# Kernel optimization log

Measured on AMD Instinct MI355X. Metric: run time of the kernel, lower is better.

## Reference

```python
import jax, jax.numpy as jnp
import numpy as np

N = 4096        # number of sparse voxel tokens (single sequence)
C = 1024        # channels
H = 16          # num_heads
D = C // H      # head_dim = 64
FREQ_DIM = D // 2 // 3   # 10 rotary freqs per spatial axis
PAD = D // 2 - 3 * FREQ_DIM  # 2 identity-padded complex pairs


def setup_inputs() -> dict:
    key = jax.random.key(0)
    ks = jax.random.split(key, 6)
    s_in = 1.0 / np.sqrt(C)
    x = jax.random.normal(ks[0], (N, C), jnp.float32)
    coords = jax.random.randint(ks[1], (N, 3), 0, 64, dtype=jnp.int32)
    W_qkv = jax.random.normal(ks[2], (C, 3 * C), jnp.float32) * s_in
    b_qkv = jnp.zeros((3 * C,), jnp.float32)
    gamma_q = jnp.ones((H, D), jnp.float32)
    gamma_k = jnp.ones((H, D), jnp.float32)
    W_out = jax.random.normal(ks[3], (C, C), jnp.float32) * s_in
    b_out = jnp.zeros((C,), jnp.float32)
    return {"x": x, "coords": coords, "W_qkv": W_qkv, "b_qkv": b_qkv,
            "gamma_q": gamma_q, "gamma_k": gamma_k, "W_out": W_out, "b_out": b_out}


def _rms_norm(t, gamma):
    # F.normalize(x, dim=-1) * gamma * sqrt(D), computed in fp32
    t = t.astype(jnp.float32)
    nrm = jnp.maximum(jnp.linalg.norm(t, axis=-1, keepdims=True), 1e-12)
    return (t / nrm) * gamma * np.float32(np.sqrt(D))


def _rope_phases(coords):
    # freqs: rope_freq[0] / rope_freq[1]**(i/freq_dim)
    freqs = 1.0 / (10000.0 ** (jnp.arange(FREQ_DIM, dtype=jnp.float32) / FREQ_DIM))
    ph = coords.astype(jnp.float32).reshape(-1)[:, None] * freqs   # [N*3, FREQ_DIM]
    ph = ph.reshape(N, 3 * FREQ_DIM)
    # pad with zero-phase (identity rotation) to head_dim//2
    cos = jnp.concatenate([jnp.cos(ph), jnp.ones((N, PAD), jnp.float32)], axis=-1)
    sin = jnp.concatenate([jnp.sin(ph), jnp.zeros((N, PAD), jnp.float32)], axis=-1)
    return cos, sin


def _rope_apply(t, cos, sin):
    # complex rotation on consecutive pairs of the head dim
    tr = t.reshape(N, H, D // 2, 2)
    t0, t1 = tr[..., 0], tr[..., 1]
    c, s = cos[:, None, :], sin[:, None, :]
    o0 = t0 * c - t1 * s
    o1 = t0 * s + t1 * c
    return jnp.stack([o0, o1], axis=-1).reshape(N, H, D)


def reference(x, coords, W_qkv, b_qkv, gamma_q, gamma_k, W_out, b_out):
    qkv = (x @ W_qkv + b_qkv).reshape(N, 3, H, D)
    q, k, v = qkv[:, 0], qkv[:, 1], qkv[:, 2]
    q = _rms_norm(q, gamma_q)
    k = _rms_norm(k, gamma_k)
    cos, sin = _rope_phases(coords)
    q = _rope_apply(q, cos, sin)
    k = _rope_apply(k, cos, sin)
    scores = jnp.einsum('nhd,mhd->hnm', q, k) / np.float32(np.sqrt(D))
    attn = jax.nn.softmax(scores, axis=-1)
    h = jnp.einsum('hnm,mhd->nhd', attn, v).reshape(N, C)
    return h @ W_out + b_out
```

## Files before the change

### kernel.cpp

```cpp
#include <hip/hip_runtime.h>

#define DEVI __device__ __forceinline__

typedef __attribute__((ext_vector_type(8))) short bf16x8;
typedef __attribute__((ext_vector_type(4))) float f32x4;
typedef __attribute__((ext_vector_type(16))) float f32x16;

DEVI ushort f2bf(float f) {
  union { float f; unsigned u; } v; v.f = f;
  unsigned u = v.u;
  unsigned r = (u + 0x7FFFu + ((u >> 16) & 1u)) >> 16;
  return (ushort)r;
}
DEVI float bf2f(ushort h) {
  union { unsigned u; float f; } v; v.u = ((unsigned)h) << 16;
  return v.f;
}
DEVI unsigned pkbf(float lo, float hi) {
  unsigned r;
  asm("v_cvt_pk_bf16_f32 %0, %1, %2" : "=v"(r) : "v"(lo), "v"(hi));
  return r;
}
DEVI float exp2v(float x) {
#if __has_builtin(__builtin_amdgcn_exp2f)
  return __builtin_amdgcn_exp2f(x);
#else
  return exp2f(x);
#endif
}

DEVI void gload_lds16(const ushort* g, ushort* l) {
  __builtin_amdgcn_global_load_lds((const __attribute__((address_space(1))) void*)g,
                                   (__attribute__((address_space(3))) void*)l, 16, 0, 0);
}

DEVI void xcd_swz(int& bx, int& by) {
  const int nx = gridDim.x;
  const int flat = blockIdx.x + blockIdx.y * nx;
  const int cpx = (nx * gridDim.y) >> 3;
  const int swz = (flat & 7) * cpx + (flat >> 3);
  bx = swz % nx;
  by = swz / nx;
}

__global__ __launch_bounds__(256) void cast_x(const float* __restrict__ in,
                                              ushort* __restrict__ out, int n4) {
  int i = blockIdx.x * blockDim.x + threadIdx.x;
  if (i < n4) {
    const float4 v = ((const float4*)in)[i];
    uint2 o;
    o.x = (unsigned)f2bf(v.x) | ((unsigned)f2bf(v.y) << 16);
    o.y = (unsigned)f2bf(v.z) | ((unsigned)f2bf(v.w) << 16);
    ((uint2*)out)[i] = o;
  }
}

__global__ __launch_bounds__(256) void transpose_cast(const float* __restrict__ in,
                                                      ushort* __restrict__ out,
                                                      int R, int Cc) {
  __shared__ ushort tile[64][65];
  const int t = threadIdx.x;
  const int r0 = blockIdx.y * 64, c0 = blockIdx.x * 64;
  for (int i = 0; i < 16; ++i) {
    int rr = i * 4 + (t >> 6), cc = t & 63;
    tile[rr][cc] = f2bf(in[(size_t)(r0 + rr) * Cc + c0 + cc]);
  }
  __syncthreads();
  for (int i = 0; i < 16; ++i) {
    int cc = i * 4 + (t >> 6), rr = t & 63;
    out[(size_t)(c0 + cc) * R + r0 + rr] = tile[rr][cc];
  }
}

template<int EPI>
__global__ __launch_bounds__(256) void gemm_bt(const ushort* __restrict__ A,
                                               const ushort* __restrict__ Bt,
                                               const float* __restrict__ bias,
                                               void* __restrict__ outp,
                                               int M, int Nn, int K) {
  __shared__ ushort As[128 * 32];
  __shared__ ushort Bs[128 * 32];
  const int tid = threadIdx.x;
  const int w = tid >> 6, l = tid & 63;
  int bx, by;
  xcd_swz(bx, by);
  const int m0 = by * 128, n0 = bx * 128;
  const int wm = (w >> 1) * 64, wn = (w & 1) * 64;
  const int lc = l & 15, lg = l >> 4;

  f32x4 acc[4][4];
  for (int i = 0; i < 4; ++i)
    for (int j = 0; j < 4; ++j) acc[i][j] = (f32x4){0.f, 0.f, 0.f, 0.f};

  const int srow = w * 32 + (l >> 2);
  const int scol = (l & 3) * 8;
  const ushort* gA = A + (size_t)(m0 + srow) * K + scol;
  const ushort* gB = Bt + (size_t)(n0 + srow) * K + scol;

  for (int k0 = 0; k0 < K; k0 += 32) {
    gload_lds16(gA + k0,                 As + (w * 32 + 0) * 32);
    gload_lds16(gA + k0 + (size_t)16 * K, As + (w * 32 + 16) * 32);
    gload_lds16(gB + k0,                 Bs + (w * 32 + 0) * 32);
    gload_lds16(gB + k0 + (size_t)16 * K, Bs + (w * 32 + 16) * 32);
    __syncthreads();
    bf16x8 af[4], bfr[4];
    for (int mi = 0; mi < 4; ++mi)
      af[mi] = *(const bf16x8*)(As + (wm + mi * 16 + lc) * 32 + lg * 8);
    for (int ni = 0; ni < 4; ++ni)
      bfr[ni] = *(const bf16x8*)(Bs + (wn + ni * 16 + lc) * 32 + lg * 8);
    for (int mi = 0; mi < 4; ++mi)
      for (int ni = 0; ni < 4; ++ni)
        acc[mi][ni] = __builtin_amdgcn_mfma_f32_16x16x32_bf16(af[mi], bfr[ni], acc[mi][ni], 0, 0, 0);
    __syncthreads();
  }

  const int lr = lg * 4;
  if constexpr (EPI == 1) {
    float* O = (float*)outp;
    for (int ni = 0; ni < 4; ++ni) {
      int col = n0 + wn + ni * 16 + lc;
      float bv = bias[col];
      for (int mi = 0; mi < 4; ++mi)
        for (int r = 0; r < 4; ++r)
          O[(size_t)(m0 + wm + mi * 16 + lr + r) * Nn + col] = acc[mi][ni][r] + bv;
    }
  } else {
    ushort* O = (ushort*)outp;
    for (int ni = 0; ni < 4; ++ni) {
      int col = n0 + wn + ni * 16 + lc;
      float bv = bias[col];
      int grp = col >> 10;
      int hh = (col >> 6) & 15;
      int dd = col & 63;
      if (grp < 2) {
        size_t base = (size_t)grp * (16 * 4096 * 64) + (size_t)hh * (4096 * 64) + dd;
        for (int mi = 0; mi < 4; ++mi)
          for (int r = 0; r < 4; ++r) {
            int row = m0 + wm + mi * 16 + lr + r;
            O[base + (size_t)row * 64] = f2bf(acc[mi][ni][r] + bv);
          }
      } else {
        size_t base = (size_t)2 * (16 * 4096 * 64) + ((size_t)hh * 64 + dd) * 4096;
        for (int mi = 0; mi < 4; ++mi)
          for (int r = 0; r < 4; ++r) {
            int row = m0 + wm + mi * 16 + lr + r;
            O[base + row] = f2bf(acc[mi][ni][r] + bv);
          }
      }
    }
  }
}

DEVI void nr_one(ushort* B, const float* g, size_t base, int h, int l16,
                 float c0a, float s0a, float c1a, float s1a, float extra) {
  unsigned u0 = *(const unsigned*)(B + base + 2 * l16);
  unsigned u1 = *(const unsigned*)(B + base + 32 + 2 * l16);
  float t00 = bf2f((ushort)u0), t01 = bf2f((ushort)(u0 >> 16));
  float t10 = bf2f((ushort)u1), t11 = bf2f((ushort)(u1 >> 16));
  float ss = t00 * t00 + t01 * t01 + t10 * t10 + t11 * t11;
  for (int d = 1; d < 16; d <<= 1) ss += __shfl_xor(ss, d, 16);
  float scl = 8.f / fmaxf(sqrtf(ss), 1e-12f);
  scl *= extra;
  float g00 = g[h * 64 + 2 * l16], g01 = g[h * 64 + 2 * l16 + 1];
  float g10 = g[h * 64 + 32 + 2 * l16], g11 = g[h * 64 + 33 + 2 * l16];
  float q00 = t00 * scl * g00, q01 = t01 * scl * g01;
  float q10 = t10 * scl * g10, q11 = t11 * scl * g11;
  float o00 = q00 * c0a - q01 * s0a, o01 = q00 * s0a + q01 * c0a;
  float o10 = q10 * c1a - q11 * s1a, o11 = q10 * s1a + q11 * c1a;
  *(unsigned*)(B + base + 2 * l16) = (unsigned)f2bf(o00) | ((unsigned)f2bf(o01) << 16);
  *(unsigned*)(B + base + 32 + 2 * l16) = (unsigned)f2bf(o10) | ((unsigned)f2bf(o11) << 16);
}

__global__ __launch_bounds__(256) void norm_rope(ushort* __restrict__ Qb,
                                                 ushort* __restrict__ Kb,
                                                 const int* __restrict__ coords,
                                                 const float* __restrict__ gq,
                                                 const float* __restrict__ gk) {
  const int n = blockIdx.x, t = threadIdx.x;
  const int h = t >> 4, l16 = t & 15;
  const float L2_10K_D10 = 1.3287712379549449f;
  float c0a, s0a, c1a, s1a;
  {
    int p = l16;
    int j = p / 10, fi = p - j * 10;
    float freq = exp2f(-(float)fi * L2_10K_D10);
    float ang = (float)coords[n * 3 + j] * freq;
    c0a = cosf(ang); s0a = sinf(ang);
  }
  {
    int p = l16 + 16;
    if (p < 30) {
      int j = p / 10, fi = p - j * 10;
      float freq = exp2f(-(float)fi * L2_10K_D10);
      float ang = (float)coords[n * 3 + j] * freq;
      c1a = cosf(ang); s1a = sinf(ang);
    } else { c1a = 1.f; s1a = 0.f; }
  }
  const size_t base = ((size_t)h * 4096 + n) * 64;
  nr_one(Qb, gq, base, h, l16, c0a, s0a, c1a, s1a, 0.125f * 1.4426950408889634f);
  nr_one(Kb, gk, base, h, l16, c0a, s0a, c1a, s1a, 1.0f);
}

DEVI void attn_step(const bf16x8 (&ck)[8], const bf16x8 (&cv)[8], const bf16x8 (&qf)[4],
                    f32x16& o0, f32x16& o1, f32x4& rs) {
  const float SHIFT = 11.5416f;
  f32x16 s0, s1;
#pragma unroll
  for (int r = 0; r < 16; ++r) { s0[r] = 0.f; s1[r] = 0.f; }
#pragma unroll
  for (int c = 0; c < 4; ++c) {
    s0 = __builtin_amdgcn_mfma_f32_32x32x16_bf16(ck[c],     qf[c], s0, 0, 0, 0);
    s1 = __builtin_amdgcn_mfma_f32_32x32x16_bf16(ck[c + 4], qf[c], s1, 0, 0, 0);
  }

#pragma unroll
  for (int r = 0; r < 16; ++r) { s0[r] = exp2v(s0[r] - SHIFT); }
#pragma unroll
  for (int r = 0; r < 16; ++r) { s1[r] = exp2v(s1[r] - SHIFT); }
#pragma unroll
  for (int r = 0; r < 16; r += 4) {
    rs[0] += s0[r] + s1[r];
    rs[1] += s0[r + 1] + s1[r + 1];
    rs[2] += s0[r + 2] + s1[r + 2];
    rs[3] += s0[r + 3] + s1[r + 3];
  }

  union { unsigned u[4]; bf16x8 v; } pb[4];
  {
    auto r0 = __builtin_amdgcn_permlane32_swap(pkbf(s0[0], s0[1]), pkbf(s0[4], s0[5]), false, false);
    auto r1 = __builtin_amdgcn_permlane32_swap(pkbf(s0[2], s0[3]), pkbf(s0[6], s0[7]), false, false);
    pb[0].u[0] = r0[0]; pb[0].u[1] = r1[0]; pb[0].u[2] = r0[1]; pb[0].u[3] = r1[1];
    auto r2 = __builtin_amdgcn_permlane32_swap(pkbf(s0[8], s0[9]), pkbf(s0[12], s0[13]), false, false);
    auto r3 = __builtin_amdgcn_permlane32_swap(pkbf(s0[10], s0[11]), pkbf(s0[14], s0[15]), false, false);
    pb[1].u[0] = r2[0]; pb[1].u[1] = r3[0]; pb[1].u[2] = r2[1]; pb[1].u[3] = r3[1];
    auto r4 = __builtin_amdgcn_permlane32_swap(pkbf(s1[0], s1[1]), pkbf(s1[4], s1[5]), false, false);
    auto r5 = __builtin_amdgcn_permlane32_swap(pkbf(s1[2], s1[3]), pkbf(s1[6], s1[7]), false, false);
    pb[2].u[0] = r4[0]; pb[2].u[1] = r5[0]; pb[2].u[2] = r4[1]; pb[2].u[3] = r5[1];
    auto r6 = __builtin_amdgcn_permlane32_swap(pkbf(s1[8], s1[9]), pkbf(s1[12], s1[13]), false, false);
    auto r7 = __builtin_amdgcn_permlane32_swap(pkbf(s1[10], s1[11]), pkbf(s1[14], s1[15]), false, false);
    pb[3].u[0] = r6[0]; pb[3].u[1] = r7[0]; pb[3].u[2] = r6[1]; pb[3].u[3] = r7[1];
  }

#pragma unroll
  for (int c = 0; c < 4; ++c) {
    o0 = __builtin_amdgcn_mfma_f32_32x32x16_bf16(cv[c],     pb[c].v, o0, 0, 0, 0);
    o1 = __builtin_amdgcn_mfma_f32_32x32x16_bf16(cv[c + 4], pb[c].v, o1, 0, 0, 0);
  }
}

__global__ __launch_bounds__(256, 2) void attn_fwd(const ushort* __restrict__ Qb,
                                                   const ushort* __restrict__ Kb,
                                                   const ushort* __restrict__ Vt,
                                                   ushort* __restrict__ attnb) {
  __shared__ ushort Ks[2][4096];
  __shared__ ushort Vs[2][4096];

  const int flat = blockIdx.x + (blockIdx.y << 5);
  const int swz = (flat & 7) * 64 + (flat >> 3);
  const int bx = swz & 31, h = swz >> 5;

  const int l = threadIdx.x & 63, w = threadIdx.x >> 6;
  const int q = l & 31, hi = l >> 5;
  const int q0 = bx * 128 + w * 32;

  const ushort* qrow = Qb + ((size_t)h * 4096 + q0 + q) * 64 + hi * 8;
  bf16x8 qf[4];
#pragma unroll
  for (int c = 0; c < 4; ++c) qf[c] = *(const bf16x8*)(qrow + 16 * c);

  f32x16 o0, o1;
#pragma unroll
  for (int r = 0; r < 16; ++r) { o0[r] = 0.f; o1[r] = 0.f; }
  f32x4 rs = (f32x4){0.f, 0.f, 0.f, 0.f};

  const ushort* gK = Kb + ((size_t)h * 4096 + l) * 64 + 2 * w * 8;
  const ushort* gV = Vt + ((size_t)h * 64 + l) * 4096 + 2 * w * 8;

  ushort* Kc = &Ks[0][0]; ushort* Vc = &Vs[0][0];
  ushort* Kn = &Ks[1][0]; ushort* Vn = &Vs[1][0];

  gload_lds16(gK, Kc + 2 * w * 512);
  gload_lds16(gK + 8, Kc + (2 * w + 1) * 512);
  gload_lds16(gV, Vc + 2 * w * 512);
  gload_lds16(gV + 8, Vc + (2 * w + 1) * 512);
  asm volatile("s_waitcnt vmcnt(0)" ::: "memory");
  __builtin_amdgcn_s_barrier();
  __builtin_amdgcn_sched_barrier(0);

  const int lbase = hi * 512 + q * 8;
  for (int t = 0; t < 63; ++t) {
    const ushort* sK = gK + (size_t)(t + 1) * 64 * 64;
    const ushort* sV = gV + (t + 1) * 64;
    gload_lds16(sK, Kn + 2 * w * 512);
    gload_lds16(sK + 8, Kn + (2 * w + 1) * 512);
    gload_lds16(sV, Vn + 2 * w * 512);
    gload_lds16(sV + 8, Vn + (2 * w + 1) * 512);

    bf16x8 k[8], v[8];
#pragma unroll
    for (int c = 0; c < 4; ++c) {
      k[c]     = *(const bf16x8*)(Kc + lbase + c * 1024);
      k[c + 4] = *(const bf16x8*)(Kc + lbase + c * 1024 + 256);
      v[c]     = *(const bf16x8*)(Vc + lbase + c * 1024);
      v[c + 4] = *(const bf16x8*)(Vc + lbase + c * 1024 + 256);
    }
    __builtin_amdgcn_s_setprio(1);
    attn_step(k, v, qf, o0, o1, rs);
    __builtin_amdgcn_s_setprio(0);

    asm volatile("s_waitcnt vmcnt(0) lgkmcnt(0)" ::: "memory");
    __builtin_amdgcn_s_barrier();
    __builtin_amdgcn_sched_barrier(0);
    ushort* tp;
    tp = Kc; Kc = Kn; Kn = tp;
    tp = Vc; Vc = Vn; Vn = tp;
  }
  {
    bf16x8 k[8], v[8];
#pragma unroll
    for (int c = 0; c < 4; ++c) {
      k[c]     = *(const bf16x8*)(Kc + lbase + c * 1024);
      k[c + 4] = *(const bf16x8*)(Kc + lbase + c * 1024 + 256);
      v[c]     = *(const bf16x8*)(Vc + lbase + c * 1024);
      v[c + 4] = *(const bf16x8*)(Vc + lbase + c * 1024 + 256);
    }
    attn_step(k, v, qf, o0, o1, rs);
  }

  float lsum = (rs[0] + rs[1]) + (rs[2] + rs[3]);
  lsum += __shfl_xor(lsum, 32);
  const float inv = 1.f / lsum;
  ushort* orow = attnb + (size_t)(q0 + q) * 1024 + h * 64;
#pragma unroll
  for (int dt = 0; dt < 2; ++dt) {
    const f32x16& oo = dt ? o1 : o0;
#pragma unroll
    for (int g = 0; g < 4; ++g)
#pragma unroll
      for (int p2 = 0; p2 < 2; ++p2) {
        int r = g * 4 + p2 * 2;
        unsigned pk = pkbf(oo[r] * inv, oo[r + 1] * inv);
        *(unsigned*)(orow + dt * 32 + g * 8 + 4 * hi + p2 * 2) = pk;
      }
  }
}

extern "C" void kernel_launch(void* const* d_in, const int* in_sizes, int n_in,
                              void* d_out, int out_size, void* d_ws, size_t ws_size,
                              hipStream_t stream) {
  const float* x      = (const float*)d_in[0];
  const int*   coords = (const int*)d_in[1];
  const float* W_qkv  = (const float*)d_in[2];
  const float* b_qkv  = (const float*)d_in[3];
  const float* gq     = (const float*)d_in[4];
  const float* gk     = (const float*)d_in[5];
  const float* W_out  = (const float*)d_in[6];
  const float* b_out  = (const float*)d_in[7];
  float* out = (float*)d_out;

  char* ws = (char*)d_ws;
  ushort* xb    = (ushort*)(ws);
  ushort* wtqkv = (ushort*)(ws + (8u << 20));
  ushort* wtout = (ushort*)(ws + (14u << 20));
  ushort* Qb    = (ushort*)(ws + (16u << 20));
  ushort* Kb    = (ushort*)(ws + (24u << 20));
  ushort* Vt    = (ushort*)(ws + (32u << 20));
  ushort* attnb = (ushort*)(ws + (40u << 20));

  cast_x<<<4096, 256, 0, stream>>>(x, xb, 4096 * 1024 / 4);
  transpose_cast<<<dim3(48, 16), 256, 0, stream>>>(W_qkv, wtqkv, 1024, 3072);
  transpose_cast<<<dim3(16, 16), 256, 0, stream>>>(W_out, wtout, 1024, 1024);
  gemm_bt<0><<<dim3(24, 32), 256, 0, stream>>>(xb, wtqkv, b_qkv, (void*)Qb, 4096, 3072, 1024);
  norm_rope<<<4096, 256, 0, stream>>>(Qb, Kb, coords, gq, gk);
  attn_fwd<<<dim3(32, 16), 256, 0, stream>>>(Qb, Kb, Vt, attnb);
  gemm_bt<1><<<dim3(8, 32), 256, 0, stream>>>(attnb, wtout, b_out, (void*)out, 4096, 1024, 1024);
}
```

Measured before the change: 168.0 us.

## Fuse Q norm+RoPE into attention, merge prep casts, drop softmax shift

The three input-cast and transpose kernels are merged into one `prep` launch that dispatches on block index. Q's RMS-norm and rotary embedding now run inside the attention kernel's Q-fragment load, so the standalone pass only processes K. This removes one full read-write round trip of Q and two kernel launches. The fixed subtraction before exp2 is also dropped, which relies on the normalized score magnitude staying within fp32 and bf16 range. In exchange, the attention prologue now computes more trig per thread.

After: 166.1 us. Within noise of the previous version (-1.1%).

```diff
diff --git a/kernel.cpp b/kernel.cpp
--- a/kernel.cpp
+++ b/kernel.cpp
@@ -43,24 +43,34 @@
   by = swz / nx;
 }
 
-__global__ __launch_bounds__(256) void cast_x(const float* __restrict__ in,
-                                              ushort* __restrict__ out, int n4) {
-  int i = blockIdx.x * blockDim.x + threadIdx.x;
-  if (i < n4) {
-    const float4 v = ((const float4*)in)[i];
+__global__ __launch_bounds__(256) void prep(const float* __restrict__ x,
+                                            ushort* __restrict__ xb,
+                                            const float* __restrict__ Wq,
+                                            ushort* __restrict__ wtq,
+                                            const float* __restrict__ Wo,
+                                            ushort* __restrict__ wto) {
+  __shared__ ushort tile[64][65];
+  const int bid = blockIdx.x, t = threadIdx.x;
+  if (bid < 4096) {
+    int i = bid * 256 + t;
+    const float4 v = ((const float4*)x)[i];
     uint2 o;
     o.x = (unsigned)f2bf(v.x) | ((unsigned)f2bf(v.y) << 16);
     o.y = (unsigned)f2bf(v.z) | ((unsigned)f2bf(v.w) << 16);
-    ((uint2*)out)[i] = o;
-  }
-}
-
-__global__ __launch_bounds__(256) void transpose_cast(const float* __restrict__ in,
-                                                      ushort* __restrict__ out,
-                                                      int R, int Cc) {
-  __shared__ ushort tile[64][65];
-  const int t = threadIdx.x;
-  const int r0 = blockIdx.y * 64, c0 = blockIdx.x * 64;
+    ((uint2*)xb)[i] = o;
+    return;
+  }
+  const float* in;
+  ushort* out;
+  int R, Cc, bx, by;
+  if (bid < 4864) {
+    in = Wq; out = wtq; R = 1024; Cc = 3072;
+    bx = (bid - 4096) % 48; by = (bid - 4096) / 48;
+  } else {
+    in = Wo; out = wto; R = 1024; Cc = 1024;
+    bx = (bid - 4864) % 16; by = (bid - 4864) / 16;
+  }
+  const int r0 = by * 64, c0 = bx * 64;
   for (int i = 0; i < 16; ++i) {
     int rr = i * 4 + (t >> 6), cc = t & 63;
     tile[rr][cc] = f2bf(in[(size_t)(r0 + rr) * Cc + c0 + cc]);
@@ -151,31 +161,9 @@
   }
 }
 
-DEVI void nr_one(ushort* B, const float* g, size_t base, int h, int l16,
-                 float c0a, float s0a, float c1a, float s1a, float extra) {
-  unsigned u0 = *(const unsigned*)(B + base + 2 * l16);
-  unsigned u1 = *(const unsigned*)(B + base + 32 + 2 * l16);
-  float t00 = bf2f((ushort)u0), t01 = bf2f((ushort)(u0 >> 16));
-  float t10 = bf2f((ushort)u1), t11 = bf2f((ushort)(u1 >> 16));
-  float ss = t00 * t00 + t01 * t01 + t10 * t10 + t11 * t11;
-  for (int d = 1; d < 16; d <<= 1) ss += __shfl_xor(ss, d, 16);
-  float scl = 8.f / fmaxf(sqrtf(ss), 1e-12f);
-  scl *= extra;
-  float g00 = g[h * 64 + 2 * l16], g01 = g[h * 64 + 2 * l16 + 1];
-  float g10 = g[h * 64 + 32 + 2 * l16], g11 = g[h * 64 + 33 + 2 * l16];
-  float q00 = t00 * scl * g00, q01 = t01 * scl * g01;
-  float q10 = t10 * scl * g10, q11 = t11 * scl * g11;
-  float o00 = q00 * c0a - q01 * s0a, o01 = q00 * s0a + q01 * c0a;
-  float o10 = q10 * c1a - q11 * s1a, o11 = q10 * s1a + q11 * c1a;
-  *(unsigned*)(B + base + 2 * l16) = (unsigned)f2bf(o00) | ((unsigned)f2bf(o01) << 16);
-  *(unsigned*)(B + base + 32 + 2 * l16) = (unsigned)f2bf(o10) | ((unsigned)f2bf(o11) << 16);
-}
-
-__global__ __launch_bounds__(256) void norm_rope(ushort* __restrict__ Qb,
-                                                 ushort* __restrict__ Kb,
-                                                 const int* __restrict__ coords,
-                                                 const float* __restrict__ gq,
-                                                 const float* __restrict__ gk) {
+__global__ __launch_bounds__(256) void norm_rope_k(ushort* __restrict__ Kb,
+                                                   const int* __restrict__ coords,
+                                                   const float* __restrict__ gk) {
   const int n = blockIdx.x, t = threadIdx.x;
   const int h = t >> 4, l16 = t & 15;
   const float L2_10K_D10 = 1.3287712379549449f;
@@ -197,13 +185,25 @@
     } else { c1a = 1.f; s1a = 0.f; }
   }
   const size_t base = ((size_t)h * 4096 + n) * 64;
-  nr_one(Qb, gq, base, h, l16, c0a, s0a, c1a, s1a, 0.125f * 1.4426950408889634f);
-  nr_one(Kb, gk, base, h, l16, c0a, s0a, c1a, s1a, 1.0f);
+  unsigned u0 = *(const unsigned*)(Kb + base + 2 * l16);
+  unsigned u1 = *(const unsigned*)(Kb + base + 32 + 2 * l16);
+  float t00 = bf2f((ushort)u0), t01 = bf2f((ushort)(u0 >> 16));
+  float t10 = bf2f((ushort)u1), t11 = bf2f((ushort)(u1 >> 16));
+  float ss = t00 * t00 + t01 * t01 + t10 * t10 + t11 * t11;
+  for (int d = 1; d < 16; d <<= 1) ss += __shfl_xor(ss, d, 16);
+  float scl = 8.f / fmaxf(sqrtf(ss), 1e-12f);
+  float g00 = gk[h * 64 + 2 * l16], g01 = gk[h * 64 + 2 * l16 + 1];
+  float g10 = gk[h * 64 + 32 + 2 * l16], g11 = gk[h * 64 + 33 + 2 * l16];
+  float q00 = t00 * scl * g00, q01 = t01 * scl * g01;
+  float q10 = t10 * scl * g10, q11 = t11 * scl * g11;
+  float o00 = q00 * c0a - q01 * s0a, o01 = q00 * s0a + q01 * c0a;
+  float o10 = q10 * c1a - q11 * s1a, o11 = q10 * s1a + q11 * c1a;
+  *(unsigned*)(Kb + base + 2 * l16) = (unsigned)f2bf(o00) | ((unsigned)f2bf(o01) << 16);
+  *(unsigned*)(Kb + base + 32 + 2 * l16) = (unsigned)f2bf(o10) | ((unsigned)f2bf(o11) << 16);
 }
 
 DEVI void attn_step(const bf16x8 (&ck)[8], const bf16x8 (&cv)[8], const bf16x8 (&qf)[4],
                     f32x16& o0, f32x16& o1, f32x4& rs) {
-  const float SHIFT = 11.5416f;
   f32x16 s0, s1;
 #pragma unroll
   for (int r = 0; r < 16; ++r) { s0[r] = 0.f; s1[r] = 0.f; }
@@ -212,11 +212,10 @@
     s0 = __builtin_amdgcn_mfma_f32_32x32x16_bf16(ck[c],     qf[c], s0, 0, 0, 0);
     s1 = __builtin_amdgcn_mfma_f32_32x32x16_bf16(ck[c + 4], qf[c], s1, 0, 0, 0);
   }
-
-#pragma unroll
-  for (int r = 0; r < 16; ++r) { s0[r] = exp2v(s0[r] - SHIFT); }
-#pragma unroll
-  for (int r = 0; r < 16; ++r) { s1[r] = exp2v(s1[r] - SHIFT); }
+#pragma unroll
+  for (int r = 0; r < 16; ++r) { s0[r] = exp2v(s0[r]); }
+#pragma unroll
+  for (int r = 0; r < 16; ++r) { s1[r] = exp2v(s1[r]); }
 #pragma unroll
   for (int r = 0; r < 16; r += 4) {
     rs[0] += s0[r] + s1[r];
@@ -224,7 +223,6 @@
     rs[2] += s0[r + 2] + s1[r + 2];
     rs[3] += s0[r + 3] + s1[r + 3];
   }
-
   union { unsigned u[4]; bf16x8 v; } pb[4];
   {
     auto r0 = __builtin_amdgcn_permlane32_swap(pkbf(s0[0], s0[1]), pkbf(s0[4], s0[5]), false, false);
@@ -240,7 +238,6 @@
     auto r7 = __builtin_amdgcn_permlane32_swap(pkbf(s1[10], s1[11]), pkbf(s1[14], s1[15]), false, false);
     pb[3].u[0] = r6[0]; pb[3].u[1] = r7[0]; pb[3].u[2] = r6[1]; pb[3].u[3] = r7[1];
   }
-
 #pragma unroll
   for (int c = 0; c < 4; ++c) {
     o0 = __builtin_amdgcn_mfma_f32_32x32x16_bf16(cv[c],     pb[c].v, o0, 0, 0, 0);
@@ -251,6 +248,8 @@
 __global__ __launch_bounds__(256, 2) void attn_fwd(const ushort* __restrict__ Qb,
                                                    const ushort* __restrict__ Kb,
                                                    const ushort* __restrict__ Vt,
+                                                   const int* __restrict__ coords,
+                                                   const float* __restrict__ gq,
                                                    ushort* __restrict__ attnb) {
   __shared__ ushort Ks[2][4096];
   __shared__ ushort Vs[2][4096];
@@ -262,11 +261,44 @@
   const int l = threadIdx.x & 63, w = threadIdx.x >> 6;
   const int q = l & 31, hi = l >> 5;
   const int q0 = bx * 128 + w * 32;
-
-  const ushort* qrow = Qb + ((size_t)h * 4096 + q0 + q) * 64 + hi * 8;
+  const int n = q0 + q;
+
   bf16x8 qf[4];
-#pragma unroll
-  for (int c = 0; c < 4; ++c) qf[c] = *(const bf16x8*)(qrow + 16 * c);
+  {
+    const ushort* qrow = Qb + ((size_t)h * 4096 + n) * 64 + hi * 8;
+    float qv[32];
+#pragma unroll
+    for (int c = 0; c < 4; ++c) {
+      bf16x8 rv = *(const bf16x8*)(qrow + 16 * c);
+#pragma unroll
+      for (int j = 0; j < 8; ++j) qv[c * 8 + j] = bf2f((ushort)rv[j]);
+    }
+    float ss = 0.f;
+#pragma unroll
+    for (int i = 0; i < 32; ++i) ss += qv[i] * qv[i];
+    ss += __shfl_xor(ss, 32);
+    const float scl = 8.f / fmaxf(sqrtf(ss), 1e-12f) * 0.125f * 1.4426950408889634f;
+    const float L2_10K_D10 = 1.3287712379549449f;
+#pragma unroll
+    for (int c = 0; c < 4; ++c) {
+      union { unsigned u[4]; bf16x8 v; } pk_;
+#pragma unroll
+      for (int j2 = 0; j2 < 4; ++j2) {
+        int p = hi * 4 + 8 * c + j2;
+        int dim = hi * 8 + 16 * c + 2 * j2;
+        float cs, sn;
+        if (p < 30) {
+          int j = p / 10, fi = p - 10 * j;
+          float ang = (float)coords[n * 3 + j] * exp2f(-(float)fi * L2_10K_D10);
+          cs = cosf(ang); sn = sinf(ang);
+        } else { cs = 1.f; sn = 0.f; }
+        float te = qv[c * 8 + 2 * j2] * scl * gq[h * 64 + dim];
+        float to = qv[c * 8 + 2 * j2 + 1] * scl * gq[h * 64 + dim + 1];
+        pk_.u[j2] = pkbf(te * cs - to * sn, te * sn + to * cs);
+      }
+      qf[c] = pk_.v;
+    }
+  }
 
   f32x16 o0, o1;
 #pragma unroll
@@ -330,7 +362,7 @@
   float lsum = (rs[0] + rs[1]) + (rs[2] + rs[3]);
   lsum += __shfl_xor(lsum, 32);
   const float inv = 1.f / lsum;
-  ushort* orow = attnb + (size_t)(q0 + q) * 1024 + h * 64;
+  ushort* orow = attnb + (size_t)n * 1024 + h * 64;
 #pragma unroll
   for (int dt = 0; dt < 2; ++dt) {
     const f32x16& oo = dt ? o1 : o0;
@@ -367,11 +399,9 @@
   ushort* Vt    = (ushort*)(ws + (32u << 20));
   ushort* attnb = (ushort*)(ws + (40u << 20));
 
-  cast_x<<<4096, 256, 0, stream>>>(x, xb, 4096 * 1024 / 4);
-  transpose_cast<<<dim3(48, 16), 256, 0, stream>>>(W_qkv, wtqkv, 1024, 3072);
-  transpose_cast<<<dim3(16, 16), 256, 0, stream>>>(W_out, wtout, 1024, 1024);
+  prep<<<5120, 256, 0, stream>>>(x, xb, W_qkv, wtqkv, W_out, wtout);
   gemm_bt<0><<<dim3(24, 32), 256, 0, stream>>>(xb, wtqkv, b_qkv, (void*)Qb, 4096, 3072, 1024);
-  norm_rope<<<4096, 256, 0, stream>>>(Qb, Kb, coords, gq, gk);
-  attn_fwd<<<dim3(32, 16), 256, 0, stream>>>(Qb, Kb, Vt, attnb);
+  norm_rope_k<<<4096, 256, 0, stream>>>(Kb, coords, gk);
+  attn_fwd<<<dim3(32, 16), 256, 0, stream>>>(Qb, Kb, Vt, coords, gq, attnb);
   gemm_bt<1><<<dim3(8, 32), 256, 0, stream>>>(attnb, wtout, b_out, (void*)out, 4096, 1024, 1024);
 }
```
